# Performance work log

Measured on AMD Instinct MI355X. Metric: run time of the kernel, lower is better.

The kernel has to match this reference:

```python
import jax, jax.numpy as jnp
import numpy as np

BATCH, LEN, N_STATE, D_MODEL = 16, 512, 64, 256
DT_MIN, DT_MAX = 1e-3, 1e-1


def setup_inputs() -> dict:
    key = jax.random.key(0)
    ks = jax.random.split(key, 8)
    log_dt = jax.random.uniform(ks[7], (1,), jnp.float32) * (np.log(DT_MAX) - np.log(DT_MIN)) + np.log(DT_MIN)
    return {
        "u": jax.random.normal(ks[0], (BATCH, LEN, D_MODEL), jnp.float32),
        "Lambda_re": jax.random.normal(ks[1], (N_STATE,), jnp.float32),
        "Lambda_im": jax.random.normal(ks[2], (N_STATE,), jnp.float32),
        "B_re": jax.random.normal(ks[3], (N_STATE,), jnp.float32),
        "B_im": jax.random.normal(ks[4], (N_STATE,), jnp.float32),
        "P_re": jax.random.normal(ks[5], (N_STATE, D_MODEL), jnp.float32),
        "P_im": jax.random.normal(ks[6], (N_STATE, D_MODEL), jnp.float32),
        "log_dt": log_dt,
    }


def reference(u, Lambda_re, Lambda_im, B_re, B_im, P_re, P_im, log_dt):
    # Diagonal (S4D-style) SSM recurrence, per-channel independent states.
    dt = jnp.exp(log_dt[0])
    Lam = Lambda_re + 1j * Lambda_im                      # (N,)
    a = jnp.exp(dt * (-jnp.exp(Lam)))                     # (N,) discrete diagonal transition
    Bd = (dt * (B_re + 1j * B_im)).astype(jnp.complex64)  # (N,)
    C = (P_re + 1j * P_im).astype(jnp.complex64)          # (N, D)
    a = a.astype(jnp.complex64)

    def step(x, u_t):
        # x: (B, N, D) complex state, u_t: (B, D) real input at this timestep
        x = a[None, :, None] * x + Bd[None, :, None] * u_t[:, None, :].astype(jnp.complex64)
        y = jnp.einsum('nd,bnd->bd', C, x)                # contract state dim
        return x, y

    x0 = jnp.zeros((u.shape[0], a.shape[0], u.shape[2]), dtype=jnp.complex64)
    _, ys = jax.lax.scan(step, x0, jnp.swapaxes(u, 0, 1))  # ys: (L, B, D)
    return jnp.swapaxes(ys, 0, 1).real                     # (B, L, D) float32
```

## Files before the change

kernel.cpp:

```cpp
#include <hip/hip_runtime.h>

#define BATCH  16
#define LEN    512
#define NSTATE 64
#define DMODEL 256
#define TB     32
#define WAVES  4

__global__ __launch_bounds__(WAVES * 64, 4)
void s4d_scan_kernel(const float* __restrict__ u,
                     const float* __restrict__ Lre_p, const float* __restrict__ Lim_p,
                     const float* __restrict__ Bre_p, const float* __restrict__ Bim_p,
                     const float* __restrict__ Pre_p, const float* __restrict__ Pim_p,
                     const float* __restrict__ logdt_p,
                     float* __restrict__ y)
{
    __shared__ float cb[WAVES][NSTATE][TB + 1];

    const int tid  = threadIdx.x;
    const int lane = tid & 63;
    const int widx = tid >> 6;
    const int wid  = blockIdx.x * WAVES + widx;
    const int b    = wid >> 8;
    const int d    = wid & 255;

    const float dt  = expf(logdt_p[0]);
    const float Lre = Lre_p[lane];
    const float Lim = Lim_p[lane];
    const float eL  = expf(Lre);
    const float wre = -eL * cosf(Lim);
    const float wim = -eL * sinf(Lim);
    const float mag = expf(dt * wre);
    const float are = mag * cosf(dt * wim);
    const float aim = mag * sinf(dt * wim);
    const float Bdre = dt * Bre_p[lane];
    const float Bdim = dt * Bim_p[lane];
    const float Pre  = Pre_p[lane * DMODEL + d];
    const float Pim  = Pim_p[lane * DMODEL + d];
    const float Gre = Pre * Bdre - Pim * Bdim;
    const float Gim = Pre * Bdim + Pim * Bdre;

    float zre = 0.f, zim = 0.f;

    const float* up = u + (size_t)b * LEN * DMODEL + d;
    float*       yp = y + (size_t)b * LEN * DMODEL + d;

    const int tl = lane & 31;
    const int h  = lane >> 5;

    for (int t0 = 0; t0 < LEN; t0 += TB) {
        const float ureg = up[(t0 + tl) * DMODEL];

        #pragma unroll
        for (int tau = 0; tau < TB; ++tau) {
            const float us = __uint_as_float(
                __builtin_amdgcn_readlane(__float_as_uint(ureg), tau));
            const float nzre = fmaf(are, zre, fmaf(-aim, zim, Gre * us));
            const float nzim = fmaf(are, zim, fmaf( aim, zre, Gim * us));
            zre = nzre;
            zim = nzim;
            cb[widx][lane][tau] = zre;
        }
        __syncthreads();

        float s = 0.f;
        #pragma unroll
        for (int j = 0; j < 32; ++j)
            s += cb[widx][32 * h + j][tl];
        s += __shfl_xor(s, 32, 64);
        if (lane < 32)
            yp[(t0 + tl) * DMODEL] = s;
        __syncthreads();
    }
}

extern "C" void kernel_launch(void* const* d_in, const int* in_sizes, int n_in,
                              void* d_out, int out_size, void* d_ws, size_t ws_size,
                              hipStream_t stream) {
    const float* u      = (const float*)d_in[0];
    const float* Lre    = (const float*)d_in[1];
    const float* Lim    = (const float*)d_in[2];
    const float* Bre    = (const float*)d_in[3];
    const float* Bim    = (const float*)d_in[4];
    const float* Pre    = (const float*)d_in[5];
    const float* Pim    = (const float*)d_in[6];
    const float* logdt  = (const float*)d_in[7];
    float* y = (float*)d_out;

    const int nblocks = (BATCH * DMODEL) / WAVES;
    s4d_scan_kernel<<<nblocks, WAVES * 64, 0, stream>>>(
        u, Lre, Lim, Bre, Bim, Pre, Pim, logdt, y);
}
```

Measured before the change: 38.14 us.

## Reduce state contributions with DPP lane ops and drop block barriers

The LDS transpose buffer, in which every lane stored each timestep's state and then summed a column, is replaced. Each timestep's state sum is now partially reduced across 8-lane groups with inline-asm DPP adds. One lane per group writes a float4 of partials to a small per-wave LDS buffer, which is then summed and combined across the half-waves with one shuffle. The block-wide __syncthreads calls are gone because each wave only touches its own LDS slice, and the next 64 timesteps of input are prefetched while the current chunk is processed. In exchange, the inline asm with s_nop hazards adds instructions to every timestep, and correctness depends on in-wave LDS ordering.

```diff
diff --git a/kernel.cpp b/kernel.cpp
--- a/kernel.cpp
+++ b/kernel.cpp
@@ -4,8 +4,29 @@
 #define LEN    512
 #define NSTATE 64
 #define DMODEL 256
-#define TB     32
 #define WAVES  4
+
+__device__ __forceinline__ float dpp_add_xor1(float x) {
+    float o;
+    asm("s_nop 1\n\t"
+        "v_add_f32_dpp %0, %1, %1 quad_perm:[1,0,3,2] row_mask:0xf bank_mask:0xf"
+        : "=v"(o) : "v"(x));
+    return o;
+}
+__device__ __forceinline__ float dpp_add_xor2(float x) {
+    float o;
+    asm("s_nop 1\n\t"
+        "v_add_f32_dpp %0, %1, %1 quad_perm:[2,3,0,1] row_mask:0xf bank_mask:0xf"
+        : "=v"(o) : "v"(x));
+    return o;
+}
+__device__ __forceinline__ float dpp_add_halfmirror(float x) {
+    float o;
+    asm("s_nop 1\n\t"
+        "v_add_f32_dpp %0, %1, %1 row_half_mirror row_mask:0xf bank_mask:0xf"
+        : "=v"(o) : "v"(x));
+    return o;
+}
 
 __global__ __launch_bounds__(WAVES * 64, 4)
 void s4d_scan_kernel(const float* __restrict__ u,
@@ -15,7 +36,7 @@
                      const float* __restrict__ logdt_p,
                      float* __restrict__ y)
 {
-    __shared__ float cb[WAVES][NSTATE][TB + 1];
+    __shared__ float red[WAVES][8][36];
 
     const int tid  = threadIdx.x;
     const int lane = tid & 63;
@@ -47,30 +68,49 @@
 
     const int tl = lane & 31;
     const int h  = lane >> 5;
+    float* const myred = &red[widx][0][0];
+    float* const wrp   = &red[widx][lane >> 3][0];
 
-    for (int t0 = 0; t0 < LEN; t0 += TB) {
-        const float ureg = up[(t0 + tl) * DMODEL];
+    float ucur = up[lane * DMODEL];
+
+    for (int m = 0; m < LEN / 64; ++m) {
+        const int mn = (m + 1) & (LEN / 64 - 1);
+        float unext = up[(mn * 64 + lane) * DMODEL];
 
         #pragma unroll
-        for (int tau = 0; tau < TB; ++tau) {
-            const float us = __uint_as_float(
-                __builtin_amdgcn_readlane(__float_as_uint(ureg), tau));
-            const float nzre = fmaf(are, zre, fmaf(-aim, zim, Gre * us));
-            const float nzim = fmaf(are, zim, fmaf( aim, zre, Gim * us));
-            zre = nzre;
-            zim = nzim;
-            cb[widx][lane][tau] = zre;
+        for (int half = 0; half < 2; ++half) {
+            #pragma unroll
+            for (int s4 = 0; s4 < 8; ++s4) {
+                float4 pack;
+                #pragma unroll
+                for (int k = 0; k < 4; ++k) {
+                    const int tau = s4 * 4 + k;
+                    const float us = __uint_as_float(
+                        __builtin_amdgcn_readlane(__float_as_uint(ucur),
+                                                  half * 32 + tau));
+                    const float nzre = fmaf(are, zre, fmaf(-aim, zim, Gre * us));
+                    const float nzim = fmaf(are, zim, fmaf( aim, zre, Gim * us));
+                    zre = nzre;
+                    zim = nzim;
+                    float s = dpp_add_xor1(zre);
+                    s = dpp_add_xor2(s);
+                    s = dpp_add_halfmirror(s);
+                    ((float*)&pack)[k] = s;
+                }
+                if ((lane & 7) == 0)
+                    *(float4*)(wrp + s4 * 4) = pack;
+            }
+
+            float s0 = myred[(4 * h + 0) * 36 + tl];
+            float s1 = myred[(4 * h + 1) * 36 + tl];
+            float s2 = myred[(4 * h + 2) * 36 + tl];
+            float s3 = myred[(4 * h + 3) * 36 + tl];
+            float s = (s0 + s1) + (s2 + s3);
+            s += __shfl_xor(s, 32, 64);
+            if (lane < 32)
+                yp[(m * 64 + half * 32 + tl) * DMODEL] = s;
         }
-        __syncthreads();
-
-        float s = 0.f;
-        #pragma unroll
-        for (int j = 0; j < 32; ++j)
-            s += cb[widx][32 * h + j][tl];
-        s += __shfl_xor(s, 32, 64);
-        if (lane < 32)
-            yp[(t0 + tl) * DMODEL] = s;
-        __syncthreads();
+        ucur = unext;
     }
 }
 
```

New measurement: 47.36 us. +24.2%, slower.
